# Kernel optimization log

Hardware: AMD Instinct MI355X
Metric: run time of the kernel (lower is better)

## Reference

```python
import jax, jax.numpy as jnp
import numpy as np

E = 8      # num_experts
A = 128    # angle feature size = input_size - 4
TGT = 3    # target size
HID = 16   # expert MLP hidden / latent / main GRU hidden
OUT = 128  # motion decoder output size
B = 64
W = 128
F = A + TGT + 1  # 132
BN_EPS = 1e-5


def _gru_layer(x, Wih, Whh, bih, bhh):
    # x: (B, T, I); Wih: (3H, I); Whh: (3H, H). PyTorch GRU equations.
    xW = jnp.einsum('bti,gi->btg', x, Wih) + bih  # precompute input gates (B,T,3H)
    H = Whh.shape[1]

    def step(h, xw):
        gh = h @ Whh.T + bhh
        ir, iz, inn = jnp.split(xw, 3, axis=-1)
        hr, hz, hn = jnp.split(gh, 3, axis=-1)
        r = jax.nn.sigmoid(ir + hr)
        z = jax.nn.sigmoid(iz + hz)
        n = jnp.tanh(inn + r * hn)
        h_new = (1.0 - z) * n + z * h
        return h_new, h_new

    h0 = jnp.zeros((x.shape[0], H), x.dtype)
    _, ys = jax.lax.scan(step, h0, jnp.swapaxes(xW, 0, 1))
    return jnp.swapaxes(ys, 0, 1)  # (B, T, H)


def _expert_mlp(x, om, w1, b1, w2, b2, g, bt):
    # Blend expert weights per-sample, then matvec; fused as one einsum (same math).
    h = jnp.einsum('bi,be,eih->bh', x, om, w1) + om @ b1
    # BatchNorm1d, training-mode batch statistics (biased variance), then ELU
    m = h.mean(0)
    v = h.var(0)
    h = jax.nn.elu(g * (h - m) * jax.lax.rsqrt(v + BN_EPS) + bt)
    return jnp.einsum('bh,be,eho->bo', h, om, w2) + om @ b2


def _forward(Local, Remote,
             gW_ih0, gW_hh0, gb_ih0, gb_hh0, gW_ih1, gW_hh1, gb_ih1, gb_hh1,
             ae_w1, ae_b1, ae_w2, ae_b2, ae_g, ae_bt,
             md_w1, md_b1, md_w2, md_b2, md_g, md_bt,
             mW_ih0, mW_hh0, mb_ih0, mb_hh0, mW_ih1, mW_hh1, mb_ih1, mb_hh1):
    Bn, Wn, _ = Local.shape
    LA = Local[..., :A]
    RA = Remote[..., :A]
    LT = Local[..., A:A + TGT]
    RT = Remote[..., A:A + TGT]
    Scale = Remote[..., A + TGT]  # (B, W)

    def gate(t):
        h = _gru_layer(t, gW_ih0, gW_hh0, gb_ih0, gb_hh0)
        h = _gru_layer(h, gW_ih1, gW_hh1, gb_ih1, gb_hh1)
        return jax.nn.softmax(h, axis=-1)

    Lo = gate(LT)  # (B, W, E)
    Ro = gate(RT)

    ZL = _expert_mlp(LA.reshape(-1, A), Lo.reshape(-1, E), ae_w1, ae_b1, ae_w2, ae_b2, ae_g, ae_bt)
    ZR = _expert_mlp(RA.reshape(-1, A), Ro.reshape(-1, E), ae_w1, ae_b1, ae_w2, ae_b2, ae_g, ae_bt)
    Z = (ZL + ZR).reshape(Bn, Wn, HID)

    Z = _gru_layer(Z, mW_ih0, mW_hh0, mb_ih0, mb_hh0)
    Z = _gru_layer(Z, mW_ih1, mW_hh1, mb_ih1, mb_hh1)
    Z = Z[:, -1]  # (B, HID)

    dec_in = jnp.concatenate([Z, Scale[:, -1:]], axis=-1)  # (B, HID+1)
    return _expert_mlp(dec_in, Ro[:, -1], md_w1, md_b1, md_w2, md_b2, md_g, md_bt)


def setup_inputs() -> dict:
    key = jax.random.key(0)
    ks = iter(jax.random.split(key, 40))

    def u(shape, bound):
        return jax.random.uniform(next(ks), shape, jnp.float32, -bound, bound)

    d = {}
    d['Local'] = jax.random.normal(next(ks), (B, W, F), jnp.float32)
    d['Remote'] = jax.random.normal(next(ks), (B, W, F), jnp.float32)

    def gru_params(pref, isz, hsz):
        bd = 1.0 / np.sqrt(hsz)
        d[pref + 'W_ih0'] = u((3 * hsz, isz), bd)
        d[pref + 'W_hh0'] = u((3 * hsz, hsz), bd)
        d[pref + 'b_ih0'] = u((3 * hsz,), bd)
        d[pref + 'b_hh0'] = u((3 * hsz,), bd)
        d[pref + 'W_ih1'] = u((3 * hsz, hsz), bd)
        d[pref + 'W_hh1'] = u((3 * hsz, hsz), bd)
        d[pref + 'b_ih1'] = u((3 * hsz,), bd)
        d[pref + 'b_hh1'] = u((3 * hsz,), bd)

    gru_params('g', TGT, E)    # gating GRU: 2 layers, hidden = num_experts
    gru_params('m', HID, HID)  # main GRU: 2 layers, hidden = 16

    def expert(pref, isz, hsz, osz):
        b1 = float(np.sqrt(6.0 / (isz * hsz)))
        b2 = float(np.sqrt(6.0 / (hsz * osz)))
        d[pref + '_w1'] = u((E, isz, hsz), b1)
        d[pref + '_b1'] = jnp.zeros((E, hsz), jnp.float32)
        d[pref + '_w2'] = u((E, hsz, osz), b2)
        d[pref + '_b2'] = jnp.zeros((E, osz), jnp.float32)
        d[pref + '_g'] = jnp.ones((hsz,), jnp.float32)
        d[pref + '_bt'] = jnp.zeros((hsz,), jnp.float32)

    expert('ae', A, HID, HID)        # angle encoder
    expert('md', HID + 1, HID, OUT)  # motion decoder
    return d


def reference(Local, Remote,
              gW_ih0, gW_hh0, gb_ih0, gb_hh0, gW_ih1, gW_hh1, gb_ih1, gb_hh1,
              ae_w1, ae_b1, ae_w2, ae_b2, ae_g, ae_bt,
              md_w1, md_b1, md_w2, md_b2, md_g, md_bt,
              mW_ih0, mW_hh0, mb_ih0, mb_hh0, mW_ih1, mW_hh1, mb_ih1, mb_hh1):
    return _forward(Local, Remote,
                    gW_ih0, gW_hh0, gb_ih0, gb_hh0, gW_ih1, gW_hh1, gb_ih1, gb_hh1,
                    ae_w1, ae_b1, ae_w2, ae_b2, ae_g, ae_bt,
                    md_w1, md_b1, md_w2, md_b2, md_g, md_bt,
                    mW_ih0, mW_hh0, mb_ih0, mb_hh0, mW_ih1, mW_hh1, mb_ih1, mb_hh1)
```

## Files before the change

kernel.cpp:

```cpp
#include <hip/hip_runtime.h>
#include <cstdint>
#include <cstddef>

#define DEV __device__ __forceinline__

typedef float f2 __attribute__((ext_vector_type(2)));

constexpr float L2E = 1.4426950408889634f;
constexpr float T2E = 2.8853900817779268f;

DEV float readlanef(float v, int l) {
    return __uint_as_float(__builtin_amdgcn_readlane(__float_as_uint(v), l));
}
DEV float fsig2(float y)  { return __builtin_amdgcn_rcpf(1.0f + __builtin_amdgcn_exp2f(-y)); }
DEV float ftanh2(float y) { return 1.0f - 2.0f * __builtin_amdgcn_rcpf(1.0f + __builtin_amdgcn_exp2f(y)); }

template<int N> DEV float rorf(float v) {
    return __uint_as_float((unsigned)__builtin_amdgcn_mov_dpp(
        (int)__float_as_uint(v), 0x120 + N, 0xF, 0xF, false));
}
DEV float swzx16(float v) {
    return __uint_as_float((unsigned)__builtin_amdgcn_ds_swizzle(
        (int)__float_as_uint(v), 0x401F));
}

constexpr size_t ACC   = 0;
constexpr size_t LO    = 128;
constexpr size_t RO    = LO + 65536;
constexpr size_t HBUF  = RO + 65536;
constexpr size_t ZLAST = HBUF + 262144;
constexpr size_t XW    = ZLAST + 1024;
constexpr size_t WS_NEED = XW + 393216;

__global__ __launch_bounds__(64, 1) void k1_gate(
    const float* __restrict__ Local, const float* __restrict__ Remote,
    const float* __restrict__ Wih0, const float* __restrict__ Whh0,
    const float* __restrict__ bih0, const float* __restrict__ bhh0,
    const float* __restrict__ Wih1, const float* __restrict__ Whh1,
    const float* __restrict__ bih1, const float* __restrict__ bhh1,
    float* __restrict__ ws)
{
    const int tid = threadIdx.x;
    const int j = tid & 7;
    const int layer = (tid >> 4) & 1;
    const int blk = blockIdx.x;
    const int track = blk >> 6;
    const int b = blk & 63;
    if (blk == 0) ws[ACC + tid] = 0.f;

    __shared__ float xwg[128][24];
    __shared__ float h1all[128][9];

    const float* __restrict__ src = track ? Remote : Local;
    for (int t = tid; t < 128; t += 64) {
        const float* p = src + ((size_t)b * 128 + t) * 132 + 128;
        float x0 = p[0], x1 = p[1], x2 = p[2];
#pragma unroll
        for (int u = 0; u < 24; ++u) {
            float a = bih0[u];
            a = fmaf(Wih0[u * 3 + 0], x0, a);
            a = fmaf(Wih0[u * 3 + 1], x1, a);
            a = fmaf(Wih0[u * 3 + 2], x2, a);
            xwg[t][u] = a * (u < 16 ? L2E : T2E);
        }
    }

    const float* __restrict__ WA = layer ? Whh1 : Whh0;
    const float mhi = layer ? 1.f : 0.f;
    const float m0f = layer ? 0.f : 1.f;
    f2 wa2r[4], wa2z[4], wa2c[4], wb2r[4], wb2z[4], wb2c[4];
#pragma unroll
    for (int m = 0; m < 4; ++m) {
        int k0 = (j - 2 * m) & 7, k1i = (j - 2 * m - 1) & 7;
        wa2r[m].x = L2E * WA[j * 8 + k0];        wa2r[m].y = L2E * WA[j * 8 + k1i];
        wa2z[m].x = L2E * WA[(8 + j) * 8 + k0];  wa2z[m].y = L2E * WA[(8 + j) * 8 + k1i];
        wa2c[m].x = T2E * WA[(16 + j) * 8 + k0]; wa2c[m].y = T2E * WA[(16 + j) * 8 + k1i];
        wb2r[m].x = mhi * L2E * Wih1[j * 8 + k0];        wb2r[m].y = mhi * L2E * Wih1[j * 8 + k1i];
        wb2z[m].x = mhi * L2E * Wih1[(8 + j) * 8 + k0];  wb2z[m].y = mhi * L2E * Wih1[(8 + j) * 8 + k1i];
        wb2c[m].x = mhi * T2E * Wih1[(16 + j) * 8 + k0]; wb2c[m].y = mhi * T2E * Wih1[(16 + j) * 8 + k1i];
    }
    const float base_r  = L2E * (layer ? (bih1[j] + bhh1[j])         : bhh0[j]);
    const float base_z  = L2E * (layer ? (bih1[8 + j] + bhh1[8 + j]) : bhh0[8 + j]);
    const float base_in = T2E * (layer ? bih1[16 + j]                : 0.f);
    const float base_dn = T2E * (layer ? bhh1[16 + j]                : bhh0[16 + j]);
    __syncthreads();

    float hown = 0.f;
    float p0 = xwg[0][j], p1 = xwg[0][8 + j], p2 = xwg[0][16 + j];
#pragma unroll 1
    for (int t = 0; t <= 128; ++t) {
        int tn = t < 127 ? t + 1 : 127;
        float q0 = xwg[tn][j], q1 = xwg[tn][8 + j], q2 = xwg[tn][16 + j];
        float b0 = swzx16(hown);
        f2 A2[4], B2[4];
        A2[0].x = hown;           A2[0].y = rorf<1>(hown);
        A2[1].x = rorf<2>(hown);  A2[1].y = rorf<3>(hown);
        A2[2].x = rorf<4>(hown);  A2[2].y = rorf<5>(hown);
        A2[3].x = rorf<6>(hown);  A2[3].y = rorf<7>(hown);
        B2[0].x = b0;             B2[0].y = rorf<1>(b0);
        B2[1].x = rorf<2>(b0);    B2[1].y = rorf<3>(b0);
        B2[2].x = rorf<4>(b0);    B2[2].y = rorf<5>(b0);
        B2[3].x = rorf<6>(b0);    B2[3].y = rorf<7>(b0);

        f2 sra = wa2r[0] * A2[0], srb = wb2r[0] * B2[0];
        f2 sza = wa2z[0] * A2[0], szb = wb2z[0] * B2[0];
        f2 sca = wa2c[0] * A2[0], scb = wb2c[0] * B2[0];
#pragma unroll
        for (int m = 1; m < 4; ++m) {
            sra += wa2r[m] * A2[m];  srb += wb2r[m] * B2[m];
            sza += wa2z[m] * A2[m];  szb += wb2z[m] * B2[m];
            sca += wa2c[m] * A2[m];  scb += wb2c[m] * B2[m];
        }
        f2 sr = sra + srb, sz = sza + szb;
        float ar = fmaf(m0f, p0, base_r) + sr.x + sr.y;
        float az = fmaf(m0f, p1, base_z) + sz.x + sz.y;
        float acA = sca.x + sca.y;
        float acB = scb.x + scb.y;
        float r = fsig2(ar);
        float z = fsig2(az);
        float in_ = layer ? (base_in + acB) : p2;
        float dn  = base_dn + acA;
        float n = ftanh2(fmaf(r, dn, in_));
        float hnew = fmaf(z, hown - n, n);
        bool act = layer ? (t >= 1) : (t < 128);
        hown = act ? hnew : hown;
        if (tid >= 16 && tid < 24) h1all[t ? t - 1 : 0][j] = hown;
        p0 = q0; p1 = q1; p2 = q2;
    }
    __syncthreads();

    float* __restrict__ outp = ws + (track ? RO : LO);
    for (int t = tid; t < 128; t += 64) {
        float vv[8];
#pragma unroll
        for (int k = 0; k < 8; ++k) vv[k] = h1all[t][k];
        float mx = vv[0];
#pragma unroll
        for (int k = 1; k < 8; ++k) mx = fmaxf(mx, vv[k]);
        float ssum = 0.f;
#pragma unroll
        for (int k = 0; k < 8; ++k) { vv[k] = __expf(vv[k] - mx); ssum += vv[k]; }
        float inv = __builtin_amdgcn_rcpf(ssum);
        size_t base = ((size_t)b * 128 + t) * 8;
        float4 o0 = make_float4(vv[0] * inv, vv[1] * inv, vv[2] * inv, vv[3] * inv);
        float4 o1 = make_float4(vv[4] * inv, vv[5] * inv, vv[6] * inv, vv[7] * inv);
        *(float4*)(outp + base) = o0;
        *(float4*)(outp + base + 4) = o1;
    }
}

__global__ __launch_bounds__(256) void k2_expert1(
    const float* __restrict__ Local, const float* __restrict__ Remote,
    const float* __restrict__ ae_w1, const float* __restrict__ ae_b1,
    float* __restrict__ ws)
{
    const int blk = blockIdx.x;
    const int track = blk >> 7;
    const int n0 = (blk & 127) * 64;
    const float* __restrict__ X = track ? Remote : Local;
    const float* __restrict__ om = ws + (track ? RO : LO);

    __shared__ __align__(16) float xsh[64 * 132];
    __shared__ __align__(16) float wsh[16 * 1060];
    __shared__ float omsh[64][8];
    __shared__ float b1sh[128];
    __shared__ float red[32];
    const int tid = threadIdx.x;

    for (int i = tid; i < 2048; i += 256) {
        int r = i >> 5, q = i & 31;
        ((float4*)&xsh[r * 132])[q] = ((const float4*)(X + (size_t)(n0 + r) * 132))[q];
    }
    for (int i4 = tid; i4 < 4096; i4 += 256) {
        float4 v = ((const float4*)ae_w1)[i4];
        int i = i4 * 4;
#pragma unroll
        for (int c = 0; c < 4; ++c) {
            int ii = i + c;
            int h = ii & 15, kk = (ii >> 4) & 127, e = ii >> 11;
            float vc = c == 0 ? v.x : c == 1 ? v.y : c == 2 ? v.z : v.w;
            wsh[h * 1060 + e * 132 + kk] = vc;
        }
    }
    for (int i = tid; i < 512; i += 256) omsh[i >> 3][i & 7] = om[(size_t)(n0 + (i >> 3)) * 8 + (i & 7)];
    for (int i = tid; i < 128; i += 256) b1sh[i] = ae_b1[i];
    if (tid < 32) red[tid] = 0.f;
    __syncthreads();

    const int hh = tid & 15, rg = tid >> 4;
    float acc[4][8];
#pragma unroll
    for (int r = 0; r < 4; ++r)
#pragma unroll
        for (int e = 0; e < 8; ++e) acc[r][e] = 0.f;

#pragma unroll 4
    for (int kq = 0; kq < 32; ++kq) {
        float4 xv[4], wv[8];
#pragma unroll
        for (int r = 0; r < 4; ++r) xv[r] = *(const float4*)&xsh[(rg * 4 + r) * 132 + kq * 4];
#pragma unroll
        for (int e = 0; e < 8; ++e) wv[e] = *(const float4*)&wsh[hh * 1060 + e * 132 + kq * 4];
#pragma unroll
        for (int r = 0; r < 4; ++r)
#pragma unroll
            for (int e = 0; e < 8; ++e) {
                float a = acc[r][e];
                a = fmaf(xv[r].x, wv[e].x, a);
                a = fmaf(xv[r].y, wv[e].y, a);
                a = fmaf(xv[r].z, wv[e].z, a);
                a = fmaf(xv[r].w, wv[e].w, a);
                acc[r][e] = a;
            }
    }

    float s = 0.f, s2 = 0.f;
    float* __restrict__ hout = ws + HBUF + (size_t)track * 131072;
#pragma unroll
    for (int r = 0; r < 4; ++r) {
        int row = rg * 4 + r;
        float hv = 0.f;
#pragma unroll
        for (int e = 0; e < 8; ++e) hv = fmaf(omsh[row][e], acc[r][e] + b1sh[e * 16 + hh], hv);
        hout[(size_t)(n0 + row) * 16 + hh] = hv;
        s += hv; s2 += hv * hv;
    }
    __syncthreads();
    atomicAdd(&red[hh], s);
    atomicAdd(&red[16 + hh], s2);
    __syncthreads();
    if (tid < 32) atomicAdd(&ws[ACC + track * 32 + tid], red[tid]);
}

__global__ __launch_bounds__(256) void k3_phaseA(
    const float* __restrict__ ae_w2, const float* __restrict__ ae_b2,
    const float* __restrict__ ae_g, const float* __restrict__ ae_bt,
    const float* __restrict__ mWih0, const float* __restrict__ mbih0,
    float* __restrict__ ws)
{
    const int blk = blockIdx.x;
    const int s = blk >> 2;
    const int r0 = (blk & 3) * 32;
    const int tid = threadIdx.x;

    __shared__ float stat[4][16];
    __shared__ __align__(16) float w2t[16 * 132];
    __shared__ float b2sh[128];
    __shared__ float omsh[2][32][8];
    __shared__ __align__(16) float actsh[2][32][16];
    __shared__ __align__(16) float zsh[32][20];
    __shared__ __align__(16) float wihsh[48][20];
    __shared__ float bihsh[48];

    if (tid < 32) {
        int trk = tid >> 4, h = tid & 15;
        float sm = ws[ACC + trk * 32 + h], s2 = ws[ACC + trk * 32 + 16 + h];
        float m = sm * (1.f / 8192.f);
        float v = fmaxf(s2 * (1.f / 8192.f) - m * m, 0.f);
        stat[trk * 2][h] = m;
        stat[trk * 2 + 1][h] = rsqrtf(v + 1e-5f);
    }
    for (int i = tid; i < 2048; i += 256) {
        int e = i >> 8, h = (i >> 4) & 15, o = i & 15;
        w2t[o * 132 + e * 16 + h] = ae_w2[i];
    }
    for (int i = tid; i < 128; i += 256) b2sh[i] = ae_b2[i];
    for (int i = tid; i < 768; i += 256) wihsh[i >> 4][i & 15] = mWih0[i];
    if (tid < 48) bihsh[tid] = mbih0[tid];
    for (int i = tid; i < 512; i += 256) {
        int trk = i >> 8, r = (i >> 3) & 31, e = i & 7;
        omsh[trk][r][e] = ws[(trk ? RO : LO) + ((size_t)s * 128 + r0 + r) * 8 + e];
    }
    __syncthreads();

    for (int i = tid; i < 1024; i += 256) {
        int trk = i >> 9, r = (i >> 4) & 31, h = i & 15;
        float v = ws[HBUF + (size_t)trk * 131072 + ((size_t)s * 128 + r0 + r) * 16 + h];
        float a = ae_g[h] * (v - stat[trk * 2][h]) * stat[trk * 2 + 1][h] + ae_bt[h];
        actsh[trk][r][h] = a > 0.f ? a : expm1f(a);
    }
    __syncthreads();

    {
        const int o = tid & 15, rb = tid >> 4;
        float zacc[2] = {0.f, 0.f};
#pragma unroll
        for (int ec = 0; ec < 2; ++ec) {
            float4 wv[4][4];
            float bo[4];
#pragma unroll
            for (int e4 = 0; e4 < 4; ++e4) {
                bo[e4] = b2sh[(ec * 4 + e4) * 16 + o];
#pragma unroll
                for (int q = 0; q < 4; ++q)
                    wv[e4][q] = *(const float4*)&w2t[o * 132 + (ec * 4 + e4) * 16 + q * 4];
            }
#pragma unroll
            for (int r2 = 0; r2 < 2; ++r2) {
                int r = rb * 2 + r2;
#pragma unroll
                for (int trk = 0; trk < 2; ++trk) {
                    float4 av[4];
#pragma unroll
                    for (int q = 0; q < 4; ++q) av[q] = *(const float4*)&actsh[trk][r][q * 4];
#pragma unroll
                    for (int e4 = 0; e4 < 4; ++e4) {
                        int e = ec * 4 + e4;
                        float t = bo[e4];
                        t = fmaf(av[0].x, wv[e4][0].x, t);
                        t = fmaf(av[0].y, wv[e4][0].y, t);
                        t = fmaf(av[0].z, wv[e4][0].z, t);
                        t = fmaf(av[0].w, wv[e4][0].w, t);
                        t = fmaf(av[1].x, wv[e4][1].x, t);
                        t = fmaf(av[1].y, wv[e4][1].y, t);
                        t = fmaf(av[1].z, wv[e4][1].z, t);
                        t = fmaf(av[1].w, wv[e4][1].w, t);
                        t = fmaf(av[2].x, wv[e4][2].x, t);
                        t = fmaf(av[2].y, wv[e4][2].y, t);
                        t = fmaf(av[2].z, wv[e4][2].z, t);
                        t = fmaf(av[2].w, wv[e4][2].w, t);
                        t = fmaf(av[3].x, wv[e4][3].x, t);
                        t = fmaf(av[3].y, wv[e4][3].y, t);
                        t = fmaf(av[3].z, wv[e4][3].z, t);
                        t = fmaf(av[3].w, wv[e4][3].w, t);
                        zacc[r2] = fmaf(omsh[trk][r][e], t, zacc[r2]);
                    }
                }
            }
        }
#pragma unroll
        for (int r2 = 0; r2 < 2; ++r2) zsh[rb * 2 + r2][o] = zacc[r2];
    }
    __syncthreads();

    {
        const int r = tid >> 3, g0 = (tid & 7) * 6;
        float4 zv[4];
#pragma unroll
        for (int q = 0; q < 4; ++q) zv[q] = *(const float4*)&zsh[r][q * 4];
        float* __restrict__ xwp = ws + XW + ((size_t)s * 128 + r0 + r) * 48;
#pragma unroll
        for (int gg = 0; gg < 6; ++gg) {
            int g = g0 + gg;
            float a = bihsh[g];
#pragma unroll
            for (int q = 0; q < 4; ++q) {
                float4 wv = *(const float4*)&wihsh[g][q * 4];
                a = fmaf(zv[q].x, wv.x, a);
                a = fmaf(zv[q].y, wv.y, a);
                a = fmaf(zv[q].z, wv.z, a);
                a = fmaf(zv[q].w, wv.w, a);
            }
            xwp[g] = a * (g < 32 ? L2E : T2E);
        }
    }
}

__global__ __launch_bounds__(64, 1) void k4_rec(
    const float* __restrict__ Whh0, const float* __restrict__ bhh0,
    const float* __restrict__ Wih1, const float* __restrict__ Whh1,
    const float* __restrict__ bih1, const float* __restrict__ bhh1,
    float* __restrict__ ws)
{
    const int s = blockIdx.x;
    const int tid = threadIdx.x;
    __shared__ __align__(16) float xwsh[128 * 48];

    const float4* __restrict__ xwg = (const float4*)(ws + XW + (size_t)s * 6144);
    for (int i = tid; i < 1536; i += 64) ((float4*)xwsh)[i] = xwg[i];

    const int j = tid & 15;
    const int layer = (tid >> 4) & 1;

    const float* __restrict__ WA = layer ? Whh1 : Whh0;
    const float mhi = layer ? 1.f : 0.f;
    const float m0f = layer ? 0.f : 1.f;
    f2 wa2r[8], wa2z[8], wa2c[8], wb2r[8], wb2z[8], wb2c[8];
#pragma unroll
    for (int m = 0; m < 8; ++m) {
        int k0 = (j - 2 * m) & 15, k1i = (j - 2 * m - 1) & 15;
        wa2r[m].x = L2E * WA[j * 16 + k0];        wa2r[m].y = L2E * WA[j * 16 + k1i];
        wa2z[m].x = L2E * WA[(16 + j) * 16 + k0]; wa2z[m].y = L2E * WA[(16 + j) * 16 + k1i];
        wa2c[m].x = T2E * WA[(32 + j) * 16 + k0]; wa2c[m].y = T2E * WA[(32 + j) * 16 + k1i];
        wb2r[m].x = mhi * L2E * Wih1[j * 16 + k0];        wb2r[m].y = mhi * L2E * Wih1[j * 16 + k1i];
        wb2z[m].x = mhi * L2E * Wih1[(16 + j) * 16 + k0]; wb2z[m].y = mhi * L2E * Wih1[(16 + j) * 16 + k1i];
        wb2c[m].x = mhi * T2E * Wih1[(32 + j) * 16 + k0]; wb2c[m].y = mhi * T2E * Wih1[(32 + j) * 16 + k1i];
    }
    const float base_r  = L2E * (layer ? (bih1[j] + bhh1[j])           : bhh0[j]);
    const float base_z  = L2E * (layer ? (bih1[16 + j] + bhh1[16 + j]) : bhh0[16 + j]);
    const float base_in = T2E * (layer ? bih1[32 + j]                  : 0.f);
    const float base_dn = T2E * (layer ? bhh1[32 + j]                  : bhh0[32 + j]);
    __syncthreads();

    float hown = 0.f;
    float p0 = xwsh[j], p1 = xwsh[16 + j], p2 = xwsh[32 + j];
#pragma unroll 1
    for (int t = 0; t <= 128; ++t) {
        int tn = (t < 127 ? t + 1 : 127) * 48;
        float q0 = xwsh[tn + j], q1 = xwsh[tn + 16 + j], q2 = xwsh[tn + 32 + j];
        float b0 = swzx16(hown);
        f2 A2[8], B2[8];
        A2[0].x = hown;            A2[0].y = rorf<1>(hown);
        A2[1].x = rorf<2>(hown);   A2[1].y = rorf<3>(hown);
        A2[2].x = rorf<4>(hown);   A2[2].y = rorf<5>(hown);
        A2[3].x = rorf<6>(hown);   A2[3].y = rorf<7>(hown);
        A2[4].x = rorf<8>(hown);   A2[4].y = rorf<9>(hown);
        A2[5].x = rorf<10>(hown);  A2[5].y = rorf<11>(hown);
        A2[6].x = rorf<12>(hown);  A2[6].y = rorf<13>(hown);
        A2[7].x = rorf<14>(hown);  A2[7].y = rorf<15>(hown);
        B2[0].x = b0;              B2[0].y = rorf<1>(b0);
        B2[1].x = rorf<2>(b0);     B2[1].y = rorf<3>(b0);
        B2[2].x = rorf<4>(b0);     B2[2].y = rorf<5>(b0);
        B2[3].x = rorf<6>(b0);     B2[3].y = rorf<7>(b0);
        B2[4].x = rorf<8>(b0);     B2[4].y = rorf<9>(b0);
        B2[5].x = rorf<10>(b0);    B2[5].y = rorf<11>(b0);
        B2[6].x = rorf<12>(b0);    B2[6].y = rorf<13>(b0);
        B2[7].x = rorf<14>(b0);    B2[7].y = rorf<15>(b0);

        f2 sra = wa2r[0] * A2[0], srb = wb2r[0] * B2[0];
        f2 sza = wa2z[0] * A2[0], szb = wb2z[0] * B2[0];
        f2 sca = wa2c[0] * A2[0], scb = wb2c[0] * B2[0];
#pragma unroll
        for (int m = 1; m < 8; ++m) {
            sra += wa2r[m] * A2[m];  srb += wb2r[m] * B2[m];
            sza += wa2z[m] * A2[m];  szb += wb2z[m] * B2[m];
            sca += wa2c[m] * A2[m];  scb += wb2c[m] * B2[m];
        }
        f2 sr = sra + srb, sz = sza + szb;
        float ar = fmaf(m0f, p0, base_r) + sr.x + sr.y;
        float az = fmaf(m0f, p1, base_z) + sz.x + sz.y;
        float acA = sca.x + sca.y;
        float acB = scb.x + scb.y;
        float r = fsig2(ar);
        float z = fsig2(az);
        float in_ = layer ? (base_in + acB) : p2;
        float dn  = base_dn + acA;
        float n = ftanh2(fmaf(r, dn, in_));
        float hnew = fmaf(z, hown - n, n);
        bool act = layer ? (t >= 1) : (t < 128);
        hown = act ? hnew : hown;
        p0 = q0; p1 = q1; p2 = q2;
    }
    if (tid >= 16 && tid < 32) ws[ZLAST + (size_t)s * 16 + j] = hown;
}

__global__ __launch_bounds__(256, 1) void k34_fused(
    const float* __restrict__ ae_w2, const float* __restrict__ ae_b2,
    const float* __restrict__ ae_g, const float* __restrict__ ae_bt,
    const float* __restrict__ mWih0, const float* __restrict__ mbih0,
    const float* __restrict__ Whh0, const float* __restrict__ bhh0,
    const float* __restrict__ Wih1, const float* __restrict__ Whh1,
    const float* __restrict__ bih1, const float* __restrict__ bhh1,
    float* __restrict__ ws)
{
    const int s = blockIdx.x;
    const int tid = threadIdx.x;

    __shared__ float stat[4][16];
    __shared__ float omsh[2][128][8];
    __shared__ __align__(16) float w2t[16 * 132];
    __shared__ float b2sh[128];
    __shared__ __align__(16) float actsh[2][128][16];
    __shared__ __align__(16) float zsh[128][20];
    __shared__ __align__(16) float wihsh[48][20];
    __shared__ float bihsh[48];
    __shared__ float xwsh[128 * 48];

    if (tid < 32) {
        int trk = tid >> 4, h = tid & 15;
        float sm = ws[ACC + trk * 32 + h], s2 = ws[ACC + trk * 32 + 16 + h];
        float m = sm * (1.f / 8192.f);
        float v = fmaxf(s2 * (1.f / 8192.f) - m * m, 0.f);
        stat[trk * 2][h] = m;
        stat[trk * 2 + 1][h] = rsqrtf(v + 1e-5f);
    }
    for (int i = tid; i < 2048; i += 256) {
        int e = i >> 8, h = (i >> 4) & 15, o = i & 15;
        w2t[o * 132 + e * 16 + h] = ae_w2[i];
    }
    for (int i = tid; i < 128; i += 256) b2sh[i] = ae_b2[i];
    for (int i = tid; i < 768; i += 256) wihsh[i >> 4][i & 15] = mWih0[i];
    if (tid < 48) bihsh[tid] = mbih0[tid];
    for (int i = tid; i < 2048; i += 256) {
        int trk = i >> 10, r = (i >> 3) & 127, e = i & 7;
        omsh[trk][r][e] = ws[(trk ? RO : LO) + ((size_t)s * 128 + r) * 8 + e];
    }
    __syncthreads();

    for (int i = tid; i < 4096; i += 256) {
        int trk = i >> 11, r = (i >> 4) & 127, h = i & 15;
        float v = ws[HBUF + (size_t)trk * 131072 + ((size_t)s * 128 + r) * 16 + h];
        float a = ae_g[h] * (v - stat[trk * 2][h]) * stat[trk * 2 + 1][h] + ae_bt[h];
        actsh[trk][r][h] = a > 0.f ? a : expm1f(a);
    }
    __syncthreads();

    {
        const int o = tid & 15, rb = tid >> 4;
        float zacc[8];
#pragma unroll
        for (int r8 = 0; r8 < 8; ++r8) zacc[r8] = 0.f;
#pragma unroll
        for (int ec = 0; ec < 2; ++ec) {
            float4 wv[4][4];
#pragma unroll
            for (int e4 = 0; e4 < 4; ++e4)
#pragma unroll
                for (int q = 0; q < 4; ++q)
                    wv[e4][q] = *(const float4*)&w2t[o * 132 + (ec * 4 + e4) * 16 + q * 4];
#pragma unroll
            for (int r8 = 0; r8 < 8; ++r8) {
                int r = rb * 8 + r8;
#pragma unroll
                for (int trk = 0; trk < 2; ++trk) {
                    float4 av[4];
#pragma unroll
                    for (int q = 0; q < 4; ++q) av[q] = *(const float4*)&actsh[trk][r][q * 4];
#pragma unroll
                    for (int e4 = 0; e4 < 4; ++e4) {
                        int e = ec * 4 + e4;
                        float t = b2sh[e * 16 + o];
                        t = fmaf(av[0].x, wv[e4][0].x, t);
                        t = fmaf(av[0].y, wv[e4][0].y, t);
                        t = fmaf(av[0].z, wv[e4][0].z, t);
                        t = fmaf(av[0].w, wv[e4][0].w, t);
                        t = fmaf(av[1].x, wv[e4][1].x, t);
                        t = fmaf(av[1].y, wv[e4][1].y, t);
                        t = fmaf(av[1].z, wv[e4][1].z, t);
                        t = fmaf(av[1].w, wv[e4][1].w, t);
                        t = fmaf(av[2].x, wv[e4][2].x, t);
                        t = fmaf(av[2].y, wv[e4][2].y, t);
                        t = fmaf(av[2].z, wv[e4][2].z, t);
                        t = fmaf(av[2].w, wv[e4][2].w, t);
                        t = fmaf(av[3].x, wv[e4][3].x, t);
                        t = fmaf(av[3].y, wv[e4][3].y, t);
                        t = fmaf(av[3].z, wv[e4][3].z, t);
                        t = fmaf(av[3].w, wv[e4][3].w, t);
                        zacc[r8] = fmaf(omsh[trk][r][e], t, zacc[r8]);
                    }
                }
            }
        }
#pragma unroll
        for (int r8 = 0; r8 < 8; ++r8) zsh[rb * 8 + r8][o] = zacc[r8];
    }
    __syncthreads();

    {
        const int r = tid >> 1, gh = (tid & 1) * 24;
        float4 zv[4];
#pragma unroll
        for (int q = 0; q < 4; ++q) zv[q] = *(const float4*)&zsh[r][q * 4];
#pragma unroll
        for (int gg = 0; gg < 24; ++gg) {
            int g = gh + gg;
            float a = bihsh[g];
#pragma unroll
            for (int q = 0; q < 4; ++q) {
                float4 wv = *(const float4*)&wihsh[g][q * 4];
                a = fmaf(zv[q].x, wv.x, a);
                a = fmaf(zv[q].y, wv.y, a);
                a = fmaf(zv[q].z, wv.z, a);
                a = fmaf(zv[q].w, wv.w, a);
            }
            xwsh[r * 48 + g] = a * (g < 32 ? L2E : T2E);
        }
    }
    __syncthreads();

    if (tid >= 64) return;

    const int j = tid & 15;
    const int layer = (tid >> 4) & 1;

    const float* __restrict__ Wlo = layer ? Wih1 : Whh0;
    const float mhi = layer ? 1.f : 0.f;
    const float m0f = layer ? 0.f : 1.f;
    f2 wr2[16], wz2[16], wc2[16];
#pragma unroll
    for (int m = 0; m < 8; ++m) {
        wr2[m].x = L2E * Wlo[j * 16 + 2 * m];
        wr2[m].y = L2E * Wlo[j * 16 + 2 * m + 1];
        wz2[m].x = L2E * Wlo[(16 + j) * 16 + 2 * m];
        wz2[m].y = L2E * Wlo[(16 + j) * 16 + 2 * m + 1];
        wc2[m].x = T2E * Wlo[(32 + j) * 16 + 2 * m];
        wc2[m].y = T2E * Wlo[(32 + j) * 16 + 2 * m + 1];
        wr2[8 + m].x = mhi * L2E * Whh1[j * 16 + 2 * m];
        wr2[8 + m].y = mhi * L2E * Whh1[j * 16 + 2 * m + 1];
        wz2[8 + m].x = mhi * L2E * Whh1[(16 + j) * 16 + 2 * m];
        wz2[8 + m].y = mhi * L2E * Whh1[(16 + j) * 16 + 2 * m + 1];
        wc2[8 + m].x = mhi * T2E * Whh1[(32 + j) * 16 + 2 * m];
        wc2[8 + m].y = mhi * T2E * Whh1[(32 + j) * 16 + 2 * m + 1];
    }
    const float base_r  = L2E * (layer ? (bih1[j] + bhh1[j])           : bhh0[j]);
    const float base_z  = L2E * (layer ? (bih1[16 + j] + bhh1[16 + j]) : bhh0[16 + j]);
    const float base_in = T2E * (layer ? bih1[32 + j]                  : 0.f);
    const float base_dn = T2E * (layer ? bhh1[32 + j]                  : bhh0[32 + j]);

    float hown = 0.f;
    float p0 = xwsh[j], p1 = xwsh[16 + j], p2 = xwsh[32 + j];
#pragma unroll 1
    for (int t = 0; t <= 128; ++t) {
        int tn = (t < 127 ? t + 1 : 127) * 48;
        float q0 = xwsh[tn + j], q1 = xwsh[tn + 16 + j], q2 = xwsh[tn + 32 + j];
        f2 vb2[16];
#pragma unroll
        for (int m = 0; m < 16; ++m) {
            vb2[m].x = readlanef(hown, 2 * m);
            vb2[m].y = readlanef(hown, 2 * m + 1);
        }
        f2 srE = wr2[0] * vb2[0], srO = wr2[1] * vb2[1];
        f2 szE = wz2[0] * vb2[0], szO = wz2[1] * vb2[1];
#pragma unroll
        for (int m = 2; m < 16; m += 2) {
            srE += wr2[m] * vb2[m];     srO += wr2[m + 1] * vb2[m + 1];
            szE += wz2[m] * vb2[m];     szO += wz2[m + 1] * vb2[m + 1];
        }
        f2 scA = wc2[0] * vb2[0], scB = wc2[1] * vb2[1];
        f2 scC = wc2[8] * vb2[8], scD = wc2[9] * vb2[9];
#pragma unroll
        for (int m = 2; m < 8; m += 2) {
            scA += wc2[m] * vb2[m];         scB += wc2[m + 1] * vb2[m + 1];
            scC += wc2[8 + m] * vb2[8 + m]; scD += wc2[9 + m] * vb2[9 + m];
        }
        f2 sr = srE + srO, sz = szE + szO;
        f2 scL = scA + scB, scH = scC + scD;
        float ar = fmaf(m0f, p0, base_r) + sr.x + sr.y;
        float az = fmaf(m0f, p1, base_z) + sz.x + sz.y;
        float ac_lo = scL.x + scL.y;
        float ac_hi = scH.x + scH.y;
        float r = fsig2(ar);
        float z = fsig2(az);
        float in_ = layer ? (base_in + ac_lo) : p2;
        float dn  = base_dn + (layer ? ac_hi : ac_lo);
        float n = ftanh2(fmaf(r, dn, in_));
        float hnew = fmaf(z, hown - n, n);
        bool act = layer ? (t >= 1) : (t < 128);
        hown = act ? hnew : hown;
        p0 = q0; p1 = q1; p2 = q2;
    }
    if (tid >= 16 && tid < 32) ws[ZLAST + (size_t)s * 16 + j] = hown;
}

__global__ __launch_bounds__(256) void k5_dec(
    const float* __restrict__ Remote,
    const float* __restrict__ md_w1, const float* __restrict__ md_b1,
    const float* __restrict__ md_g, const float* __restrict__ md_bt,
    const float* __restrict__ md_w2, const float* __restrict__ md_b2,
    const float* __restrict__ ws, float* __restrict__ out)
{
    const int o0 = blockIdx.x * 8;
    const int tid = threadIdx.x;
    __shared__ float xsh[64][17];
    __shared__ float omsh[64][8];
    __shared__ float w1sh[2176];
    __shared__ float b1sh[128];
    __shared__ float hsh[64][17];
    __shared__ float ssum[16], ss2[16], mstat[2][16];
    __shared__ float ash[64][17];
    __shared__ float w2sh[8][16][8];
    __shared__ float b2sh[8][8];

    for (int i = tid; i < 1024; i += 256) xsh[i >> 4][i & 15] = ws[ZLAST + i];
    if (tid < 64) xsh[tid][16] = Remote[((size_t)tid * 128 + 127) * 132 + 131];
    for (int i = tid; i < 512; i += 256)
        omsh[i >> 3][i & 7] = ws[RO + ((size_t)(i >> 3) * 128 + 127) * 8 + (i & 7)];
    for (int i = tid; i < 2176; i += 256) w1sh[i] = md_w1[i];
    for (int i = tid; i < 128; i += 256) b1sh[i] = md_b1[i];
    for (int i = tid; i < 1024; i += 256) {
        int e = i >> 7, h = (i >> 3) & 15, oo = i & 7;
        w2sh[e][h][oo] = md_w2[((size_t)e * 16 + h) * 128 + o0 + oo];
    }
    if (tid < 64) b2sh[tid >> 3][tid & 7] = md_b2[(size_t)(tid >> 3) * 128 + o0 + (tid & 7)];
    if (tid < 16) { ssum[tid] = 0.f; ss2[tid] = 0.f; }
    __syncthreads();

    for (int i = tid; i < 1024; i += 256) {
        int b = i >> 4, h = i & 15;
        float accv = 0.f;
#pragma unroll
        for (int e = 0; e < 8; ++e) {
            float t = b1sh[e * 16 + h];
            const float* w = &w1sh[e * 272 + h];
#pragma unroll
            for (int i2 = 0; i2 < 17; ++i2) t = fmaf(xsh[b][i2], w[i2 * 16], t);
            accv = fmaf(omsh[b][e], t, accv);
        }
        hsh[b][h] = accv;
        atomicAdd(&ssum[h], accv);
        atomicAdd(&ss2[h], accv * accv);
    }
    __syncthreads();
    if (tid < 16) {
        float m = ssum[tid] * (1.f / 64.f);
        float v = fmaxf(ss2[tid] * (1.f / 64.f) - m * m, 0.f);
        mstat[0][tid] = m;
        mstat[1][tid] = rsqrtf(v + 1e-5f);
    }
    __syncthreads();
    for (int i = tid; i < 1024; i += 256) {
        int b = i >> 4, h = i & 15;
        float a = md_g[h] * (hsh[b][h] - mstat[0][h]) * mstat[1][h] + md_bt[h];
        ash[b][h] = a > 0.f ? a : expm1f(a);
    }
    __syncthreads();

    for (int i = tid; i < 512; i += 256) {
        int b = i >> 3, oo = i & 7;
        float accv = 0.f;
#pragma unroll
        for (int e = 0; e < 8; ++e) {
            float t = b2sh[e][oo];
#pragma unroll
            for (int h = 0; h < 16; ++h) t = fmaf(ash[b][h], w2sh[e][h][oo], t);
            accv = fmaf(omsh[b][e], t, accv);
        }
        out[(size_t)b * 128 + o0 + oo] = accv;
    }
}

extern "C" void kernel_launch(void* const* d_in, const int* in_sizes, int n_in,
                              void* d_out, int out_size, void* d_ws, size_t ws_size,
                              hipStream_t stream) {
    const float* Local  = (const float*)d_in[0];
    const float* Remote = (const float*)d_in[1];
    const float* gWih0  = (const float*)d_in[2];
    const float* gWhh0  = (const float*)d_in[3];
    const float* gbih0  = (const float*)d_in[4];
    const float* gbhh0  = (const float*)d_in[5];
    const float* gWih1  = (const float*)d_in[6];
    const float* gWhh1  = (const float*)d_in[7];
    const float* gbih1  = (const float*)d_in[8];
    const float* gbhh1  = (const float*)d_in[9];
    const float* mWih0  = (const float*)d_in[10];
    const float* mWhh0  = (const float*)d_in[11];
    const float* mbih0  = (const float*)d_in[12];
    const float* mbhh0  = (const float*)d_in[13];
    const float* mWih1  = (const float*)d_in[14];
    const float* mWhh1  = (const float*)d_in[15];
    const float* mbih1  = (const float*)d_in[16];
    const float* mbhh1  = (const float*)d_in[17];
    const float* ae_w1  = (const float*)d_in[18];
    const float* ae_b1  = (const float*)d_in[19];
    const float* ae_w2  = (const float*)d_in[20];
    const float* ae_b2  = (const float*)d_in[21];
    const float* ae_g   = (const float*)d_in[22];
    const float* ae_bt  = (const float*)d_in[23];
    const float* md_w1  = (const float*)d_in[24];
    const float* md_b1  = (const float*)d_in[25];
    const float* md_w2  = (const float*)d_in[26];
    const float* md_b2  = (const float*)d_in[27];
    const float* md_g   = (const float*)d_in[28];
    const float* md_bt  = (const float*)d_in[29];
    float* ws  = (float*)d_ws;
    float* out = (float*)d_out;

    k1_gate<<<128, 64, 0, stream>>>(Local, Remote, gWih0, gWhh0, gbih0, gbhh0,
                                    gWih1, gWhh1, gbih1, gbhh1, ws);
    k2_expert1<<<256, 256, 0, stream>>>(Local, Remote, ae_w1, ae_b1, ws);
    if (ws_size >= WS_NEED * sizeof(float)) {
        k3_phaseA<<<256, 256, 0, stream>>>(ae_w2, ae_b2, ae_g, ae_bt, mWih0, mbih0, ws);
        k4_rec<<<64, 64, 0, stream>>>(mWhh0, mbhh0, mWih1, mWhh1, mbih1, mbhh1, ws);
    } else {
        k34_fused<<<64, 256, 0, stream>>>(ae_w2, ae_b2, ae_g, ae_bt, mWih0, mbih0,
                                          mWhh0, mbhh0, mWih1, mWhh1, mbih1, mbhh1, ws);
    }
    k5_dec<<<16, 256, 0, stream>>>(Remote, md_w1, md_b1, md_g, md_bt,
                                   md_w2, md_b2, ws, out);
}
```

Baseline: 229.6 us.

## Transpose GRU input-gate buffers and unroll recurrence by four with float4 prefetch

The precomputed input-gate activations for both the gate GRU and the main GRU are now stored gate-major (transposed, rows padded to 140), so each lane fetches four timesteps with one float4 load. The recurrent loops are unrolled by four with a two-chunk register prefetch, and the main GRU reads directly from global memory instead of first staging all of it into shared memory. The per-step swizzle now runs at the end of each step, and extra zero padding is written so that reads past the last step stay defined. This targets per-step LDS load latency on the serial recurrence critical path, at the cost of more registers, a larger workspace, and reliance on global memory or cache latency being hidden by the prefetch.

Result: faster. 218.4 us (-4.9%).

```diff
diff --git a/kernel.cpp b/kernel.cpp
--- a/kernel.cpp
+++ b/kernel.cpp
@@ -29,8 +29,8 @@
 constexpr size_t RO    = LO + 65536;
 constexpr size_t HBUF  = RO + 65536;
 constexpr size_t ZLAST = HBUF + 262144;
-constexpr size_t XW    = ZLAST + 1024;
-constexpr size_t WS_NEED = XW + 393216;
+constexpr size_t XWT   = ZLAST + 1024;
+constexpr size_t WS_NEED = XWT + 430080;
 
 __global__ __launch_bounds__(64, 1) void k1_gate(
     const float* __restrict__ Local, const float* __restrict__ Remote,
@@ -48,7 +48,7 @@
     const int b = blk & 63;
     if (blk == 0) ws[ACC + tid] = 0.f;
 
-    __shared__ float xwg[128][24];
+    __shared__ __align__(16) float xwgT[24 * 140];
     __shared__ float h1all[128][9];
 
     const float* __restrict__ src = track ? Remote : Local;
@@ -61,9 +61,10 @@
             a = fmaf(Wih0[u * 3 + 0], x0, a);
             a = fmaf(Wih0[u * 3 + 1], x1, a);
             a = fmaf(Wih0[u * 3 + 2], x2, a);
-            xwg[t][u] = a * (u < 16 ? L2E : T2E);
-        }
-    }
+            xwgT[u * 140 + t] = a * (u < 16 ? L2E : T2E);
+        }
+    }
+    for (int i = tid; i < 96; i += 64) xwgT[(i >> 2) * 140 + 128 + (i & 3)] = 0.f;
 
     const float* __restrict__ WA = layer ? Whh1 : Whh0;
     const float mhi = layer ? 1.f : 0.f;
@@ -85,47 +86,62 @@
     const float base_dn = T2E * (layer ? bhh1[16 + j]                : bhh0[16 + j]);
     __syncthreads();
 
-    float hown = 0.f;
-    float p0 = xwg[0][j], p1 = xwg[0][8 + j], p2 = xwg[0][16 + j];
+    float hown = 0.f, b0 = 0.f;
+    float4 d0 = *(const float4*)&xwgT[j * 140];
+    float4 d1 = *(const float4*)&xwgT[(8 + j) * 140];
+    float4 d2 = *(const float4*)&xwgT[(16 + j) * 140];
+    float4 n0v = *(const float4*)&xwgT[j * 140 + 4];
+    float4 n1v = *(const float4*)&xwgT[(8 + j) * 140 + 4];
+    float4 n2v = *(const float4*)&xwgT[(16 + j) * 140 + 4];
 #pragma unroll 1
-    for (int t = 0; t <= 128; ++t) {
-        int tn = t < 127 ? t + 1 : 127;
-        float q0 = xwg[tn][j], q1 = xwg[tn][8 + j], q2 = xwg[tn][16 + j];
-        float b0 = swzx16(hown);
-        f2 A2[4], B2[4];
-        A2[0].x = hown;           A2[0].y = rorf<1>(hown);
-        A2[1].x = rorf<2>(hown);  A2[1].y = rorf<3>(hown);
-        A2[2].x = rorf<4>(hown);  A2[2].y = rorf<5>(hown);
-        A2[3].x = rorf<6>(hown);  A2[3].y = rorf<7>(hown);
-        B2[0].x = b0;             B2[0].y = rorf<1>(b0);
-        B2[1].x = rorf<2>(b0);    B2[1].y = rorf<3>(b0);
-        B2[2].x = rorf<4>(b0);    B2[2].y = rorf<5>(b0);
-        B2[3].x = rorf<6>(b0);    B2[3].y = rorf<7>(b0);
-
-        f2 sra = wa2r[0] * A2[0], srb = wb2r[0] * B2[0];
-        f2 sza = wa2z[0] * A2[0], szb = wb2z[0] * B2[0];
-        f2 sca = wa2c[0] * A2[0], scb = wb2c[0] * B2[0];
-#pragma unroll
-        for (int m = 1; m < 4; ++m) {
-            sra += wa2r[m] * A2[m];  srb += wb2r[m] * B2[m];
-            sza += wa2z[m] * A2[m];  szb += wb2z[m] * B2[m];
-            sca += wa2c[m] * A2[m];  scb += wb2c[m] * B2[m];
-        }
-        f2 sr = sra + srb, sz = sza + szb;
-        float ar = fmaf(m0f, p0, base_r) + sr.x + sr.y;
-        float az = fmaf(m0f, p1, base_z) + sz.x + sz.y;
-        float acA = sca.x + sca.y;
-        float acB = scb.x + scb.y;
-        float r = fsig2(ar);
-        float z = fsig2(az);
-        float in_ = layer ? (base_in + acB) : p2;
-        float dn  = base_dn + acA;
-        float n = ftanh2(fmaf(r, dn, in_));
-        float hnew = fmaf(z, hown - n, n);
-        bool act = layer ? (t >= 1) : (t < 128);
-        hown = act ? hnew : hown;
-        if (tid >= 16 && tid < 24) h1all[t ? t - 1 : 0][j] = hown;
-        p0 = q0; p1 = q1; p2 = q2;
+    for (int tc = 0; tc < 33; ++tc) {
+        float4 e0 = d0, e1 = d1, e2 = d2;
+        d0 = n0v; d1 = n1v; d2 = n2v;
+        int nc = tc + 2; if (nc > 32) nc = 32;
+        n0v = *(const float4*)&xwgT[j * 140 + nc * 4];
+        n1v = *(const float4*)&xwgT[(8 + j) * 140 + nc * 4];
+        n2v = *(const float4*)&xwgT[(16 + j) * 140 + nc * 4];
+#pragma unroll
+        for (int tt = 0; tt < 4; ++tt) {
+            const int t = tc * 4 + tt;
+            float p0 = tt == 0 ? e0.x : tt == 1 ? e0.y : tt == 2 ? e0.z : e0.w;
+            float p1 = tt == 0 ? e1.x : tt == 1 ? e1.y : tt == 2 ? e1.z : e1.w;
+            float p2 = tt == 0 ? e2.x : tt == 1 ? e2.y : tt == 2 ? e2.z : e2.w;
+            f2 A2[4], B2[4];
+            A2[0].x = hown;           A2[0].y = rorf<1>(hown);
+            A2[1].x = rorf<2>(hown);  A2[1].y = rorf<3>(hown);
+            A2[2].x = rorf<4>(hown);  A2[2].y = rorf<5>(hown);
+            A2[3].x = rorf<6>(hown);  A2[3].y = rorf<7>(hown);
+            B2[0].x = b0;             B2[0].y = rorf<1>(b0);
+            B2[1].x = rorf<2>(b0);    B2[1].y = rorf<3>(b0);
+            B2[2].x = rorf<4>(b0);    B2[2].y = rorf<5>(b0);
+            B2[3].x = rorf<6>(b0);    B2[3].y = rorf<7>(b0);
+
+            f2 sra = wa2r[0] * A2[0], srb = wb2r[0] * B2[0];
+            f2 sza = wa2z[0] * A2[0], szb = wb2z[0] * B2[0];
+            f2 sca = wa2c[0] * A2[0], scb = wb2c[0] * B2[0];
+#pragma unroll
+            for (int m = 1; m < 4; ++m) {
+                sra += wa2r[m] * A2[m];  srb += wb2r[m] * B2[m];
+                sza += wa2z[m] * A2[m];  szb += wb2z[m] * B2[m];
+                sca += wa2c[m] * A2[m];  scb += wb2c[m] * B2[m];
+            }
+            f2 sr = sra + srb, sz = sza + szb;
+            float ar = fmaf(m0f, p0, base_r) + sr.x + sr.y;
+            float az = fmaf(m0f, p1, base_z) + sz.x + sz.y;
+            float acA = sca.x + sca.y;
+            float acB = scb.x + scb.y;
+            float r = fsig2(ar);
+            float z = fsig2(az);
+            float in_ = layer ? (base_in + acB) : p2;
+            float dn  = base_dn + acA;
+            float n = ftanh2(fmaf(r, dn, in_));
+            float hnew = fmaf(z, hown - n, n);
+            bool act = layer ? (t >= 1 && t < 129) : (t < 128);
+            hown = act ? hnew : hown;
+            if (t >= 1 && t < 129 && tid >= 16 && tid < 24) h1all[t - 1][j] = hown;
+            b0 = swzx16(hown);
+        }
     }
     __syncthreads();
 
@@ -334,14 +350,14 @@
     __syncthreads();
 
     {
-        const int r = tid >> 3, g0 = (tid & 7) * 6;
+        const int r = tid & 31, gi = tid >> 5;
         float4 zv[4];
 #pragma unroll
         for (int q = 0; q < 4; ++q) zv[q] = *(const float4*)&zsh[r][q * 4];
-        float* __restrict__ xwp = ws + XW + ((size_t)s * 128 + r0 + r) * 48;
+        float* __restrict__ xwp = ws + XWT + (size_t)s * 6720 + (size_t)(r0 + r);
 #pragma unroll
         for (int gg = 0; gg < 6; ++gg) {
-            int g = g0 + gg;
+            int g = gi * 6 + gg;
             float a = bihsh[g];
 #pragma unroll
             for (int q = 0; q < 4; ++q) {
@@ -351,7 +367,14 @@
                 a = fmaf(zv[q].z, wv.z, a);
                 a = fmaf(zv[q].w, wv.w, a);
             }
-            xwp[g] = a * (g < 32 ? L2E : T2E);
+            xwp[(size_t)g * 140] = a * (g < 32 ? L2E : T2E);
+        }
+        if (r0 == 96 && r < 4) {
+#pragma unroll
+            for (int gg = 0; gg < 6; ++gg) {
+                int g = gi * 6 + gg;
+                ws[XWT + (size_t)s * 6720 + (size_t)g * 140 + 128 + r] = 0.f;
+            }
         }
     }
 }
@@ -364,11 +387,6 @@
 {
     const int s = blockIdx.x;
     const int tid = threadIdx.x;
-    __shared__ __align__(16) float xwsh[128 * 48];
-
-    const float4* __restrict__ xwg = (const float4*)(ws + XW + (size_t)s * 6144);
-    for (int i = tid; i < 1536; i += 64) ((float4*)xwsh)[i] = xwg[i];
-
     const int j = tid & 15;
     const int layer = (tid >> 4) & 1;
 
@@ -390,56 +408,76 @@
     const float base_z  = L2E * (layer ? (bih1[16 + j] + bhh1[16 + j]) : bhh0[16 + j]);
     const float base_in = T2E * (layer ? bih1[32 + j]                  : 0.f);
     const float base_dn = T2E * (layer ? bhh1[32 + j]                  : bhh0[32 + j]);
-    __syncthreads();
-
-    float hown = 0.f;
-    float p0 = xwsh[j], p1 = xwsh[16 + j], p2 = xwsh[32 + j];
+
+    const float* __restrict__ xwb = ws + XWT + (size_t)s * 6720;
+    const float* __restrict__ r0p = xwb + (size_t)j * 140;
+    const float* __restrict__ r1p = xwb + (size_t)(16 + j) * 140;
+    const float* __restrict__ r2p = xwb + (size_t)(32 + j) * 140;
+
+    float4 d0 = *(const float4*)(r0p);
+    float4 d1 = *(const float4*)(r1p);
+    float4 d2 = *(const float4*)(r2p);
+    float4 n0v = *(const float4*)(r0p + 4);
+    float4 n1v = *(const float4*)(r1p + 4);
+    float4 n2v = *(const float4*)(r2p + 4);
+
+    float hown = 0.f, b0 = 0.f;
 #pragma unroll 1
-    for (int t = 0; t <= 128; ++t) {
-        int tn = (t < 127 ? t + 1 : 127) * 48;
-        float q0 = xwsh[tn + j], q1 = xwsh[tn + 16 + j], q2 = xwsh[tn + 32 + j];
-        float b0 = swzx16(hown);
-        f2 A2[8], B2[8];
-        A2[0].x = hown;            A2[0].y = rorf<1>(hown);
-        A2[1].x = rorf<2>(hown);   A2[1].y = rorf<3>(hown);
-        A2[2].x = rorf<4>(hown);   A2[2].y = rorf<5>(hown);
-        A2[3].x = rorf<6>(hown);   A2[3].y = rorf<7>(hown);
-        A2[4].x = rorf<8>(hown);   A2[4].y = rorf<9>(hown);
-        A2[5].x = rorf<10>(hown);  A2[5].y = rorf<11>(hown);
-        A2[6].x = rorf<12>(hown);  A2[6].y = rorf<13>(hown);
-        A2[7].x = rorf<14>(hown);  A2[7].y = rorf<15>(hown);
-        B2[0].x = b0;              B2[0].y = rorf<1>(b0);
-        B2[1].x = rorf<2>(b0);     B2[1].y = rorf<3>(b0);
-        B2[2].x = rorf<4>(b0);     B2[2].y = rorf<5>(b0);
-        B2[3].x = rorf<6>(b0);     B2[3].y = rorf<7>(b0);
-        B2[4].x = rorf<8>(b0);     B2[4].y = rorf<9>(b0);
-        B2[5].x = rorf<10>(b0);    B2[5].y = rorf<11>(b0);
-        B2[6].x = rorf<12>(b0);    B2[6].y = rorf<13>(b0);
-        B2[7].x = rorf<14>(b0);    B2[7].y = rorf<15>(b0);
-
-        f2 sra = wa2r[0] * A2[0], srb = wb2r[0] * B2[0];
-        f2 sza = wa2z[0] * A2[0], szb = wb2z[0] * B2[0];
-        f2 sca = wa2c[0] * A2[0], scb = wb2c[0] * B2[0];
-#pragma unroll
-        for (int m = 1; m < 8; ++m) {
-            sra += wa2r[m] * A2[m];  srb += wb2r[m] * B2[m];
-            sza += wa2z[m] * A2[m];  szb += wb2z[m] * B2[m];
-            sca += wa2c[m] * A2[m];  scb += wb2c[m] * B2[m];
-        }
-        f2 sr = sra + srb, sz = sza + szb;
-        float ar = fmaf(m0f, p0, base_r) + sr.x + sr.y;
-        float az = fmaf(m0f, p1, base_z) + sz.x + sz.y;
-        float acA = sca.x + sca.y;
-        float acB = scb.x + scb.y;
-        float r = fsig2(ar);
-        float z = fsig2(az);
-        float in_ = layer ? (base_in + acB) : p2;
-        float dn  = base_dn + acA;
-        float n = ftanh2(fmaf(r, dn, in_));
-        float hnew = fmaf(z, hown - n, n);
-        bool act = layer ? (t >= 1) : (t < 128);
-        hown = act ? hnew : hown;
-        p0 = q0; p1 = q1; p2 = q2;
+    for (int tc = 0; tc < 33; ++tc) {
+        float4 e0 = d0, e1 = d1, e2 = d2;
+        d0 = n0v; d1 = n1v; d2 = n2v;
+        int nc = tc + 2; if (nc > 32) nc = 32;
+        n0v = *(const float4*)(r0p + nc * 4);
+        n1v = *(const float4*)(r1p + nc * 4);
+        n2v = *(const float4*)(r2p + nc * 4);
+#pragma unroll
+        for (int tt = 0; tt < 4; ++tt) {
+            const int t = tc * 4 + tt;
+            float p0 = tt == 0 ? e0.x : tt == 1 ? e0.y : tt == 2 ? e0.z : e0.w;
+            float p1 = tt == 0 ? e1.x : tt == 1 ? e1.y : tt == 2 ? e1.z : e1.w;
+            float p2 = tt == 0 ? e2.x : tt == 1 ? e2.y : tt == 2 ? e2.z : e2.w;
+            f2 A2[8], B2[8];
+            A2[0].x = hown;            A2[0].y = rorf<1>(hown);
+            A2[1].x = rorf<2>(hown);   A2[1].y = rorf<3>(hown);
+            A2[2].x = rorf<4>(hown);   A2[2].y = rorf<5>(hown);
+            A2[3].x = rorf<6>(hown);   A2[3].y = rorf<7>(hown);
+            A2[4].x = rorf<8>(hown);   A2[4].y = rorf<9>(hown);
+            A2[5].x = rorf<10>(hown);  A2[5].y = rorf<11>(hown);
+            A2[6].x = rorf<12>(hown);  A2[6].y = rorf<13>(hown);
+            A2[7].x = rorf<14>(hown);  A2[7].y = rorf<15>(hown);
+            B2[0].x = b0;              B2[0].y = rorf<1>(b0);
+            B2[1].x = rorf<2>(b0);     B2[1].y = rorf<3>(b0);
+            B2[2].x = rorf<4>(b0);     B2[2].y = rorf<5>(b0);
+            B2[3].x = rorf<6>(b0);     B2[3].y = rorf<7>(b0);
+            B2[4].x = rorf<8>(b0);     B2[4].y = rorf<9>(b0);
+            B2[5].x = rorf<10>(b0);    B2[5].y = rorf<11>(b0);
+            B2[6].x = rorf<12>(b0);    B2[6].y = rorf<13>(b0);
+            B2[7].x = rorf<14>(b0);    B2[7].y = rorf<15>(b0);
+
+            f2 sra = wa2r[0] * A2[0], srb = wb2r[0] * B2[0];
+            f2 sza = wa2z[0] * A2[0], szb = wb2z[0] * B2[0];
+            f2 sca = wa2c[0] * A2[0], scb = wb2c[0] * B2[0];
+#pragma unroll
+            for (int m = 1; m < 8; ++m) {
+                sra += wa2r[m] * A2[m];  srb += wb2r[m] * B2[m];
+                sza += wa2z[m] * A2[m];  szb += wb2z[m] * B2[m];
+                sca += wa2c[m] * A2[m];  scb += wb2c[m] * B2[m];
+            }
+            f2 sr = sra + srb, sz = sza + szb;
+            float ar = fmaf(m0f, p0, base_r) + sr.x + sr.y;
+            float az = fmaf(m0f, p1, base_z) + sz.x + sz.y;
+            float acA = sca.x + sca.y;
+            float acB = scb.x + scb.y;
+            float r = fsig2(ar);
+            float z = fsig2(az);
+            float in_ = layer ? (base_in + acB) : p2;
+            float dn  = base_dn + acA;
+            float n = ftanh2(fmaf(r, dn, in_));
+            float hnew = fmaf(z, hown - n, n);
+            bool act = layer ? (t >= 1 && t < 129) : (t < 128);
+            hown = act ? hnew : hown;
+            b0 = swzx16(hown);
+        }
     }
     if (tid >= 16 && tid < 32) ws[ZLAST + (size_t)s * 16 + j] = hown;
 }
```
